# Optimization experiments

Measured on AMD Instinct MI355X. Metric: run time of the kernel, lower is better.

Reference implementation:

```python
import jax, jax.numpy as jnp
import numpy as np

H = 8          # heads
C = 128        # out_channels per head (hidden_dim)
EMB = 256      # embedding_dim
NG = 64        # number of graphs in batch
EPS_LN = 1e-5


def _layer_norm(x, g, b):
    mu = x.mean(-1, keepdims=True)
    var = ((x - mu) ** 2).mean(-1, keepdims=True)
    return (x - mu) * jax.lax.rsqrt(var + EPS_LN) * g + b


def _transformer_conv(x, src, dst, Wq, bq, Wk, bk, Wv, bv, Ws, bs, Wb):
    # PyG TransformerConv, heads=H, concat=False, beta=True, root_weight=True
    N = x.shape[0]
    q = (x @ Wq + bq).reshape(N, H, C)
    k = (x @ Wk + bk).reshape(N, H, C)
    v = (x @ Wv + bv).reshape(N, H, C)
    # per-edge attention logits: q_i . k_j / sqrt(C)   (i=dst, j=src)
    logits = jnp.einsum('ehc,ehc->eh', q[dst], k[src]) / jnp.sqrt(jnp.asarray(C, x.dtype))
    # segment softmax over incoming edges of each dst node
    m = jax.ops.segment_max(logits, dst, num_segments=N)
    m = jnp.where(jnp.isfinite(m), m, 0.0)
    ex = jnp.exp(logits - m[dst])
    den = jax.ops.segment_sum(ex, dst, num_segments=N)
    alpha = ex / (den[dst] + 1e-16)                      # [E,H]
    msg = alpha[:, :, None] * v[src]                     # [E,H,C]
    out = jax.ops.segment_sum(msg, dst, num_segments=N)  # [N,H,C]
    out = out.mean(axis=1)                               # concat=False -> head mean
    # beta-gated skip connection
    x_r = x @ Ws + bs                                    # [N,C]
    beta = jax.nn.sigmoid(jnp.concatenate([out, x_r, out - x_r], axis=-1) @ Wb)  # [N,1]
    return beta * x_r + (1.0 - beta) * out


def _lin(k, fan_in, fan_out, scale=None):
    s = scale if scale is not None else 1.0 / np.sqrt(fan_in)
    k1, k2 = jax.random.split(k)
    W = jax.random.uniform(k1, (fan_in, fan_out), jnp.float32, -s, s)
    b = jax.random.uniform(k2, (fan_out,), jnp.float32, -s, s)
    return W, b


def setup_inputs() -> dict:
    key = jax.random.key(0)
    ks = jax.random.split(key, 32)
    N, E, V = 50000, 400000, 10000
    inp = {
        'x': jax.random.randint(ks[0], (N,), 0, V, jnp.int32),
        'edge_index': jax.random.randint(ks[1], (2, E), 0, N, jnp.int32),
        'batch': jnp.sort(jax.random.randint(ks[2], (N,), 0, NG, jnp.int32)),
        'emb_w': jax.random.normal(ks[3], (V, EMB), jnp.float32),
    }
    ki = 4
    for l, din in enumerate([EMB, C]):
        Wq, bq = _lin(ks[ki], din, H * C); ki += 1
        Wk, bk = _lin(ks[ki], din, H * C); ki += 1
        Wv, bv = _lin(ks[ki], din, H * C); ki += 1
        Ws, bs = _lin(ks[ki], din, C); ki += 1
        Wb, _ = _lin(ks[ki], 3 * C, 1); ki += 1
        inp.update({f'Wq{l}': Wq, f'bq{l}': bq, f'Wk{l}': Wk, f'bk{l}': bk,
                    f'Wv{l}': Wv, f'bv{l}': bv, f'Ws{l}': Ws, f'bs{l}': bs,
                    f'Wb{l}': Wb, f'g{l}': jnp.ones((C,), jnp.float32),
                    f'be{l}': jnp.zeros((C,), jnp.float32)})
    Wc1, bc1 = _lin(ks[ki], C, C // 2); ki += 1
    Wc2, bc2 = _lin(ks[ki], C // 2, 1); ki += 1
    inp.update({'Wc1': Wc1, 'bc1': bc1, 'Wc2': Wc2, 'bc2': bc2})
    return inp


def reference(x, edge_index, batch, emb_w,
              Wq0, bq0, Wk0, bk0, Wv0, bv0, Ws0, bs0, Wb0, g0, be0,
              Wq1, bq1, Wk1, bk1, Wv1, bv1, Ws1, bs1, Wb1, g1, be1,
              Wc1, bc1, Wc2, bc2):
    src, dst = edge_index[0], edge_index[1]
    h = emb_w[x]                                           # [N, EMB]
    # layer 0 (no residual, per original `if i > 0`)
    h = _transformer_conv(h, src, dst, Wq0, bq0, Wk0, bk0, Wv0, bv0, Ws0, bs0, Wb0)
    h = jax.nn.relu(_layer_norm(h, g0, be0))               # dropout = identity (eval)
    # layer 1 (residual)
    res = h
    h = _transformer_conv(h, src, dst, Wq1, bq1, Wk1, bk1, Wv1, bv1, Ws1, bs1, Wb1)
    h = jax.nn.relu(_layer_norm(h + res, g1, be1))
    # global mean pool over graphs
    s = jax.ops.segment_sum(h, batch, num_segments=NG)     # [NG, C]
    cnt = jax.ops.segment_sum(jnp.ones((h.shape[0],), h.dtype), batch, num_segments=NG)
    pooled = s / jnp.maximum(cnt, 1.0)[:, None]
    # classifier MLP
    z = jax.nn.relu(pooled @ Wc1 + bc1)
    return z @ Wc2 + bc2                                   # [NG, 1]
```

## Files before the change

### kernel.cpp

```cpp
#include <hip/hip_runtime.h>
#include <hip/hip_fp16.h>
#include <math.h>

#define HEADS 8
#define CDIM 128
#define HC 1024
#define EMBD 256
#define NGRAPH 64
#define QSCALE 0.08838834764831845f
#define QSCALE2 0.12751744f

typedef unsigned short u16;
typedef short s8v __attribute__((ext_vector_type(8)));
typedef float f4v __attribute__((ext_vector_type(4)));
typedef _Float16 h2v __attribute__((ext_vector_type(2)));

__device__ __forceinline__ float b2f(u16 u) {
  union { unsigned int i; float f; } v; v.i = ((unsigned int)u) << 16; return v.f;
}
__device__ __forceinline__ u16 f2b(float f) {
  union { float f; unsigned int i; } v; v.f = f;
  unsigned int i = v.i;
  unsigned int r = (i + 0x7FFFu + ((i >> 16) & 1u)) >> 16;
  return (u16)r;
}
__device__ __forceinline__ u16 f2h(float f) {
  __half h = __float2half(f);
  return *(u16*)&h;
}

union U4H { uint4 u; h2v h[4]; };

__global__ __launch_bounds__(256) void embed_kernel(
    const int* __restrict__ x, const float* __restrict__ emb,
    u16* __restrict__ h0, int N)
{
  int idx = blockIdx.x * 256 + threadIdx.x;
  if (idx >= N * (EMBD / 4)) return;
  int n = idx >> 6;
  int j = (idx & 63) * 4;
  int vid = x[n];
  float4 f = *(const float4*)&emb[(size_t)vid * EMBD + j];
  ushort4 u;
  u.x = f2b(f.x); u.y = f2b(f.y); u.z = f2b(f.z); u.w = f2b(f.w);
  *(ushort4*)&h0[(size_t)n * EMBD + j] = u;
}

__global__ __launch_bounds__(256) void build_WsT_swz(
    const float* __restrict__ in, u16* __restrict__ out, int K)
{
  const int KS = K / 32;
  int nt = blockIdx.x;
  int ks = blockIdx.y;
  int t = threadIdx.x;
  int lane = t & 63, ni = t >> 6;
  int q4 = lane >> 4, cn = lane & 15;
  int colL = nt * 64 + ni * 16 + cn;
  int kbase = ks * 32 + q4 * 8;
  u16 tmp[8];
#pragma unroll
  for (int e8 = 0; e8 < 8; e8++) tmp[e8] = f2b(in[(size_t)(kbase + e8) * CDIM + colL]);
  size_t base = ((((size_t)nt * KS + ks) * 4 + ni) * 64 + lane) * 8;
  *(uint4*)&out[base] = *(uint4*)tmp;
}

__global__ __launch_bounds__(256) void build_qkvT_swz(
    const float* __restrict__ Wq, const float* __restrict__ Wk, const float* __restrict__ Wv,
    u16* __restrict__ WT, int K, int hpc)
{
  __shared__ u16 tile[64][130];
  const int KS = K / 32;
  int rg0 = blockIdx.x * 128;
  int kk0 = blockIdx.y * 64;
  int chunkCols = hpc * 384;
  int chunk = rg0 / chunkCols;
  int within = rg0 - chunk * chunkCols;
  int head = chunk * hpc + within / 384;
  int sub = within % 384;
  int sect = sub >> 7;
  const float* W = (sect == 0) ? Wq : (sect == 1 ? Wk : Wv);
  float scale = (sect == 0) ? QSCALE2 : 1.0f;
  int cc0 = head * CDIM;
  int t = threadIdx.x;
  int ci = t & 127, k2 = t >> 7;
#pragma unroll
  for (int ii = 0; ii < 32; ii++) {
    int ki = k2 + ii * 2;
    tile[ki][ci] = f2b(W[(size_t)(kk0 + ki) * HC + cc0 + ci] * scale);
  }
  __syncthreads();

  int lane = t & 63, ni = t >> 6;
  int q4 = lane >> 4, cn = lane & 15;
  int ntBase = rg0 >> 6;
#pragma unroll
  for (int ntd = 0; ntd < 2; ntd++) {
#pragma unroll
    for (int ksd = 0; ksd < 2; ksd++) {
      int colL = ntd * 64 + ni * 16 + cn;
      int kL = ksd * 32 + q4 * 8;
      u16 tmp[8];
#pragma unroll
      for (int e8 = 0; e8 < 8; e8++) tmp[e8] = tile[kL + e8][colL];
      size_t base = ((((size_t)(ntBase + ntd) * KS + (kk0 >> 5) + ksd) * 4 + ni) * 64 + lane) * 8;
      *(uint4*)&WT[base] = *(uint4*)tmp;
    }
  }
}
__global__ __launch_bounds__(256) void build_qkvb(
    const float* __restrict__ bq, const float* __restrict__ bk, const float* __restrict__ bv,
    float* __restrict__ bT, int hpc)
{
  int rg = blockIdx.x * 256 + threadIdx.x;
  if (rg >= 3 * HC) return;
  int chunkCols = hpc * 384;
  int chunk = rg / chunkCols;
  int within = rg - chunk * chunkCols;
  int head = chunk * hpc + within / 384;
  int sub = within % 384;
  int sect = sub >> 7;
  int cc = head * CDIM + (sub & 127);
  bT[rg] = (sect == 0) ? bq[cc] * QSCALE2 : (sect == 1 ? bk[cc] : bv[cc]);
}

__global__ __launch_bounds__(256) void deg_kernel(const int* __restrict__ ei, int* __restrict__ deg, int E) {
  int e = blockIdx.x * 256 + threadIdx.x;
  if (e < E) atomicAdd(&deg[ei[E + e]], 1);
}
__global__ __launch_bounds__(256) void scan1_kernel(const int* __restrict__ deg, int* __restrict__ row_ptr,
                                                    int* __restrict__ bsum, int N) {
  __shared__ int sb[256];
  int t = threadIdx.x, idx = blockIdx.x * 256 + t;
  int x = (idx < N) ? deg[idx] : 0;
  sb[t] = x; __syncthreads();
  for (int off = 1; off < 256; off <<= 1) {
    int y = (t >= off) ? sb[t - off] : 0;
    __syncthreads(); sb[t] += y; __syncthreads();
  }
  if (idx < N) row_ptr[idx + 1] = sb[t];
  if (t == 255) bsum[blockIdx.x] = sb[255];
  if (idx == 0) row_ptr[0] = 0;
}
__global__ __launch_bounds__(256) void scan2_kernel(int* __restrict__ bsum, int B) {
  __shared__ int sb[256];
  int t = threadIdx.x;
  int x = (t < B) ? bsum[t] : 0;
  sb[t] = x; __syncthreads();
  for (int off = 1; off < 256; off <<= 1) {
    int y = (t >= off) ? sb[t - off] : 0;
    __syncthreads(); sb[t] += y; __syncthreads();
  }
  if (t < B) bsum[t] = sb[t] - x;
}
__global__ __launch_bounds__(256) void scan3_kernel(int* __restrict__ row_ptr, const int* __restrict__ bsum, int N) {
  int idx = blockIdx.x * 256 + threadIdx.x;
  if (idx < N) row_ptr[idx + 1] += bsum[idx >> 8];
}
__global__ __launch_bounds__(256) void scatter_kernel(const int* __restrict__ ei,
                                                      const int* __restrict__ row_ptr,
                                                      int* __restrict__ fill, int* __restrict__ col, int E) {
  int e = blockIdx.x * 256 + threadIdx.x;
  if (e >= E) return;
  int d = ei[E + e];
  int pos = row_ptr[d] + atomicAdd(&fill[d], 1);
  col[pos] = ei[e];
}
__global__ void gb_kernel(const int* __restrict__ batch, int* __restrict__ gb, int N) {
  int g = threadIdx.x;
  if (g > NGRAPH) return;
  int lo = 0, hi = N;
  while (lo < hi) { int mid = (lo + hi) >> 1; if (batch[mid] < g) lo = mid + 1; else hi = mid; }
  gb[g] = lo;
}

template <int K, int F16OUT>
__global__ __launch_bounds__(256, 3) void gemm_lds(
    const u16* __restrict__ A, const u16* __restrict__ Bswz, int col0tile,
    const float* __restrict__ bias, u16* __restrict__ outT,
    int M, int Ncol)
{
  const int LDK = K + 8;
  const int KS = K / 32;
  __shared__ __align__(16) u16 As[64 * LDK];
  int t = threadIdx.x, lane = t & 63, w = t >> 6;
  int q4 = lane >> 4, cn = lane & 15;
  int m0 = blockIdx.y * 64;
  int ntL = blockIdx.x * 4 + w;
  bool wActive = ntL * 64 < Ncol;
  int ntG = col0tile + ntL;

  if (m0 + 64 <= M) {
    const u16* Ablk = A + (size_t)m0 * K;
#pragma unroll
    for (int ii = 0; ii < K / 32; ii++) {
      int g = (ii * 256 + t) * 8;
      int r = g / K, c = g - r * K;
      *(uint4*)&As[r * LDK + c] = *(const uint4*)(Ablk + g);
    }
  } else {
#pragma unroll
    for (int ii = 0; ii < K / 32; ii++) {
      int g = (ii * 256 + t) * 8;
      int r = g / K, c = g - r * K;
      int gr = m0 + r; if (gr >= M) gr = M - 1;
      *(uint4*)&As[r * LDK + c] = *(const uint4*)(A + (size_t)gr * K + c);
    }
  }
  __syncthreads();

  if (!wActive) return;

  f4v acc[4][4] = {};
  const u16* bb = Bswz + ((size_t)ntG * KS * 4) * 64 * 8 + lane * 8;
#pragma unroll
  for (int ks = 0; ks < KS; ks++) {
    s8v bf[4], af[4];
#pragma unroll
    for (int ni = 0; ni < 4; ni++)
      bf[ni] = *(const s8v*)(bb + ((size_t)ks * 4 + ni) * 64 * 8);
#pragma unroll
    for (int mi = 0; mi < 4; mi++)
      af[mi] = *(const s8v*)&As[(mi * 16 + cn) * LDK + ks * 32 + q4 * 8];
#pragma unroll
    for (int mi = 0; mi < 4; mi++)
#pragma unroll
      for (int ni = 0; ni < 4; ni++)
        acc[mi][ni] = __builtin_amdgcn_mfma_f32_16x16x32_bf16(af[mi], bf[ni], acc[mi][ni], 0, 0, 0);
  }

  u16* obase = outT + (size_t)ntL * M * 64;
  float bv[4];
#pragma unroll
  for (int ni = 0; ni < 4; ni++) bv[ni] = bias[ntG * 64 + ni * 16 + cn];
#pragma unroll
  for (int mi = 0; mi < 4; mi++) {
#pragma unroll
    for (int j = 0; j < 4; j++) {
      int gm = m0 + mi * 16 + q4 * 4 + j;
      if (gm < M) {
#pragma unroll
        for (int ni = 0; ni < 4; ni++) {
          float val = acc[mi][ni][j] + bv[ni];
          obase[(size_t)gm * 64 + ni * 16 + cn] = F16OUT ? f2h(val) : f2b(val);
        }
      }
    }
  }
}

template <int HPC>
__global__ __launch_bounds__(256) void attn_chunk_kernel(
    const u16* __restrict__ qkv,
    const int* __restrict__ row_ptr, const int* __restrict__ col,
    float* __restrict__ outacc, int N, int first)
{
  int t = threadIdx.x;
  int w = t >> 6, lane = t & 63;
  int g = lane >> 4, i = lane & 15;
  int n, j;
  if (HPC == 4)      { n = blockIdx.x;                 j = w; }
  else if (HPC == 2) { n = blockIdx.x * 2 + (w >> 1);  j = w & 1; }
  else               { n = blockIdx.x * 4 + w;         j = 0; }
  bool active = (HPC == 4) ? true : (n < N);

  int itile = i >> 3, ioff = (i & 7) * 8;
  const u16* qb = qkv + (size_t)(j * 6 + 0 + itile) * N * 64 + ioff;
  const u16* kb = qkv + (size_t)(j * 6 + 2 + itile) * N * 64 + ioff;
  const u16* vb = qkv + (size_t)(j * 6 + 4 + itile) * N * 64 + ioff;

  float acc[8] = {};
  float m = -INFINITY, l = 0.f;
  if (active) {
    U4H qu; qu.u = *(const uint4*)(qb + (size_t)n * 64);
    int e0 = row_ptr[n], e1 = row_ptr[n + 1];
    for (int eb = e0; eb < e1; eb += 8) {
      int egA = eb + g, egB = eb + 4 + g;
      bool vA = egA < e1, vB = egB < e1;
      int sA = col[vA ? egA : e1 - 1];
      int sB = col[vB ? egB : e1 - 1];
      U4H kuA, vuA, kuB, vuB;
      kuA.u = *(const uint4*)(kb + (size_t)sA * 64);
      kuB.u = *(const uint4*)(kb + (size_t)sB * 64);
      vuA.u = *(const uint4*)(vb + (size_t)sA * 64);
      vuB.u = *(const uint4*)(vb + (size_t)sB * 64);

      float pA, pB;
#if defined(__has_builtin) && __has_builtin(__builtin_amdgcn_fdot2)
      pA = __builtin_amdgcn_fdot2(kuA.h[0], qu.h[0], 0.f, false);
      pA = __builtin_amdgcn_fdot2(kuA.h[1], qu.h[1], pA, false);
      pA = __builtin_amdgcn_fdot2(kuA.h[2], qu.h[2], pA, false);
      pA = __builtin_amdgcn_fdot2(kuA.h[3], qu.h[3], pA, false);
      pB = __builtin_amdgcn_fdot2(kuB.h[0], qu.h[0], 0.f, false);
      pB = __builtin_amdgcn_fdot2(kuB.h[1], qu.h[1], pB, false);
      pB = __builtin_amdgcn_fdot2(kuB.h[2], qu.h[2], pB, false);
      pB = __builtin_amdgcn_fdot2(kuB.h[3], qu.h[3], pB, false);
#else
      pA = 0.f; pB = 0.f;
#pragma unroll
      for (int z = 0; z < 4; z++) {
        pA += (float)kuA.h[z][0] * (float)qu.h[z][0] + (float)kuA.h[z][1] * (float)qu.h[z][1];
        pB += (float)kuB.h[z][0] * (float)qu.h[z][0] + (float)kuB.h[z][1] * (float)qu.h[z][1];
      }
#endif
#pragma unroll
      for (int off = 1; off <= 8; off <<= 1) {
        pA += __shfl_xor(pA, off, 64);
        pB += __shfl_xor(pB, off, 64);
      }
      if (!vA) pA = -INFINITY;
      if (!vB) pB = -INFINITY;

      {
        float pm = fmaxf(pA, __shfl_xor(pA, 16));
        pm = fmaxf(pm, __shfl_xor(pm, 32));
        if (pm > m) {
          float al = exp2f(m - pm);
          l *= al;
#pragma unroll
          for (int z = 0; z < 8; z++) acc[z] *= al;
          m = pm;
        }
        float pe = exp2f(pA - m);
        float ps = pe + __shfl_xor(pe, 16);
        ps += __shfl_xor(ps, 32);
        l += ps;
#pragma unroll
        for (int z = 0; z < 4; z++) {
          acc[2 * z]     = fmaf(pe, (float)vuA.h[z][0], acc[2 * z]);
          acc[2 * z + 1] = fmaf(pe, (float)vuA.h[z][1], acc[2 * z + 1]);
        }
      }
      {
        float pm = fmaxf(pB, __shfl_xor(pB, 16));
        pm = fmaxf(pm, __shfl_xor(pm, 32));
        if (pm > m) {
          float al = exp2f(m - pm);
          l *= al;
#pragma unroll
          for (int z = 0; z < 8; z++) acc[z] *= al;
          m = pm;
        }
        float pe = exp2f(pB - m);
        float ps = pe + __shfl_xor(pe, 16);
        ps += __shfl_xor(ps, 32);
        l += ps;
#pragma unroll
        for (int z = 0; z < 4; z++) {
          acc[2 * z]     = fmaf(pe, (float)vuB.h[z][0], acc[2 * z]);
          acc[2 * z + 1] = fmaf(pe, (float)vuB.h[z][1], acc[2 * z + 1]);
        }
      }
    }
  }
  float inv = 0.125f / (l + 1e-16f);
#pragma unroll
  for (int z = 0; z < 8; z++) {
    float a = acc[z] * inv;
    a += __shfl_xor(a, 16);
    a += __shfl_xor(a, 32);
    acc[z] = a;
  }

  if (HPC == 1) {
    if (active && g == 0) {
      float* op = outacc + (size_t)n * CDIM + i * 8;
      if (first) {
        *(float4*)op       = make_float4(acc[0], acc[1], acc[2], acc[3]);
        *(float4*)(op + 4) = make_float4(acc[4], acc[5], acc[6], acc[7]);
      } else {
        float4 o0 = *(float4*)op, o1 = *(float4*)(op + 4);
        *(float4*)op       = make_float4(o0.x + acc[0], o0.y + acc[1], o0.z + acc[2], o0.w + acc[3]);
        *(float4*)(op + 4) = make_float4(o1.x + acc[4], o1.y + acc[5], o1.z + acc[6], o1.w + acc[7]);
      }
    }
  } else {
    __shared__ float sacc[4][128];
    if (g == 0) {
      *(float4*)&sacc[w][i * 8]     = make_float4(acc[0], acc[1], acc[2], acc[3]);
      *(float4*)&sacc[w][i * 8 + 4] = make_float4(acc[4], acc[5], acc[6], acc[7]);
    }
    __syncthreads();
    if (HPC == 4) {
      if (t < 128) {
        float v = sacc[0][t] + sacc[1][t] + sacc[2][t] + sacc[3][t];
        size_t o = (size_t)blockIdx.x * CDIM + t;
        outacc[o] = first ? v : (outacc[o] + v);
      }
    } else {
      int nn = blockIdx.x * 2 + (t >> 7);
      int c = t & 127;
      if (nn < N) {
        float v = sacc[(t >> 7) * 2][c] + sacc[(t >> 7) * 2 + 1][c];
        size_t o = (size_t)nn * CDIM + c;
        outacc[o] = first ? v : (outacc[o] + v);
      }
    }
  }
}

template <int LAYER>
__global__ __launch_bounds__(256) void epilogue_kernel(
    const float* __restrict__ outacc, const u16* __restrict__ xrT,
    const float* __restrict__ Wb, const float* __restrict__ gam, const float* __restrict__ bet,
    const u16* __restrict__ res,
    u16* __restrict__ hout,
    float* __restrict__ houtf,
    int N)
{
  int t = threadIdx.x;
  int local = t >> 7, c = t & 127, w = t >> 6;
  int n = blockIdx.x * 2 + local;
  bool act = n < N;
  __shared__ float sred[8];
  __shared__ float smv[2][3];

  float oc = 0.f, xc = 0.f;
  if (act) {
    oc = outacc[(size_t)n * CDIM + c];
    xc = b2f(xrT[((size_t)(c >> 6) * N + n) * 64 + (c & 63)]);
  }
  float pb = oc * Wb[c] + xc * Wb[CDIM + c] + (oc - xc) * Wb[2 * CDIM + c];
#pragma unroll
  for (int off = 32; off; off >>= 1) pb += __shfl_down(pb, off, 64);
  if ((t & 63) == 0) sred[w] = pb;
  __syncthreads();
  if (t == 0)   smv[0][0] = 1.f / (1.f + __expf(-(sred[0] + sred[1])));
  if (t == 128) smv[1][0] = 1.f / (1.f + __expf(-(sred[2] + sred[3])));
  __syncthreads();
  float beta = smv[local][0];
  float val = beta * xc + (1.f - beta) * oc;
  if (LAYER == 1 && act) val += b2f(res[(size_t)n * CDIM + c]);

  float s1 = val, s2 = val * val;
#pragma unroll
  for (int off = 32; off; off >>= 1) {
    s1 += __shfl_down(s1, off, 64);
    s2 += __shfl_down(s2, off, 64);
  }
  __syncthreads();
  if ((t & 63) == 0) { sred[w * 2] = s1; sred[w * 2 + 1] = s2; }
  __syncthreads();
  if (t == 0) {
    float S1 = sred[0] + sred[2], S2 = sred[1] + sred[3];
    float mu = S1 * (1.f / CDIM);
    float var = fmaxf(S2 * (1.f / CDIM) - mu * mu, 0.f);
    smv[0][1] = mu; smv[0][2] = 1.f / sqrtf(var + 1e-5f);
  }
  if (t == 128) {
    float S1 = sred[4] + sred[6], S2 = sred[5] + sred[7];
    float mu = S1 * (1.f / CDIM);
    float var = fmaxf(S2 * (1.f / CDIM) - mu * mu, 0.f);
    smv[1][1] = mu; smv[1][2] = 1.f / sqrtf(var + 1e-5f);
  }
  __syncthreads();
  if (act) {
    float y = (val - smv[local][1]) * smv[local][2] * gam[c] + bet[c];
    y = fmaxf(y, 0.f);
    if (LAYER == 0) hout[(size_t)n * CDIM + c] = f2b(y);
    else            houtf[(size_t)n * CDIM + c] = y;
  }
}

__global__ __launch_bounds__(256) void classifier_kernel(
    const float* __restrict__ hf, const int* __restrict__ gb,
    const float* __restrict__ Wc1, const float* __restrict__ bc1,
    const float* __restrict__ Wc2, const float* __restrict__ bc2,
    float* __restrict__ out)
{
  int g = blockIdx.x, t = threadIdx.x;
  int half = t >> 7, c = t & 127;
  int s = gb[g], e = gb[g + 1];
  float acc = 0.f;
  for (int n = s + half; n < e; n += 2) acc += hf[(size_t)n * CDIM + c];
  __shared__ float sb[2][128];
  __shared__ float sp[128], sz[64];
  sb[half][c] = acc;
  __syncthreads();
  float cg = fmaxf((float)(e - s), 1.f);
  if (t < 128) sp[t] = (sb[0][t] + sb[1][t]) / cg;
  __syncthreads();
  if (t < 64) {
    float a = bc1[t];
    for (int cc = 0; cc < 128; cc++) a += sp[cc] * Wc1[cc * 64 + t];
    sz[t] = fmaxf(a, 0.f);
  }
  __syncthreads();
  if (t < 64) {
    float pbv = sz[t] * Wc2[t];
    for (int off = 32; off; off >>= 1) pbv += __shfl_down(pbv, off, 64);
    if (t == 0) out[g] = pbv + bc2[0];
  }
}

extern "C" void kernel_launch(void* const* d_in, const int* in_sizes, int n_in,
                              void* d_out, int out_size, void* d_ws, size_t ws_size,
                              hipStream_t stream)
{
  if (n_in != 30) return;

  const int N = in_sizes[0];
  const int E = in_sizes[1] / 2;

  const int* x     = (const int*)d_in[0];
  const int* ei    = (const int*)d_in[1];
  const int* batch = (const int*)d_in[2];
  const float* emb = (const float*)d_in[3];
  const float* Wq0 = (const float*)d_in[4];  const float* bq0 = (const float*)d_in[5];
  const float* Wk0 = (const float*)d_in[6];  const float* bk0 = (const float*)d_in[7];
  const float* Wv0 = (const float*)d_in[8];  const float* bv0 = (const float*)d_in[9];
  const float* Ws0 = (const float*)d_in[10]; const float* bs0 = (const float*)d_in[11];
  const float* Wb0 = (const float*)d_in[12]; const float* g0  = (const float*)d_in[13]; const float* be0 = (const float*)d_in[14];
  const float* Wq1 = (const float*)d_in[15]; const float* bq1 = (const float*)d_in[16];
  const float* Wk1 = (const float*)d_in[17]; const float* bk1 = (const float*)d_in[18];
  const float* Wv1 = (const float*)d_in[19]; const float* bv1 = (const float*)d_in[20];
  const float* Ws1 = (const float*)d_in[21]; const float* bs1 = (const float*)d_in[22];
  const float* Wb1 = (const float*)d_in[23]; const float* g1  = (const float*)d_in[24]; const float* be1 = (const float*)d_in[25];
  const float* Wc1 = (const float*)d_in[26]; const float* bc1 = (const float*)d_in[27];
  const float* Wc2 = (const float*)d_in[28]; const float* bc2 = (const float*)d_in[29];

  auto rnd = [](size_t b) { return (b + 511) & ~(size_t)511; };
  size_t fixedBytes =
      rnd((size_t)N * CDIM * 4) +
      rnd((size_t)N * EMBD * 2) +
      rnd((size_t)N * CDIM * 2) * 2 +
      rnd((size_t)3 * HC * EMBD * 2) +
      rnd((size_t)3 * HC * CDIM * 2) +
      rnd((size_t)3 * HC * 4) * 2 +
      rnd((size_t)CDIM * EMBD * 2) +
      rnd((size_t)CDIM * CDIM * 2) +
      rnd((size_t)N * 4) * 2 +
      rnd((size_t)(N + 1) * 4) +
      rnd((size_t)E * 4) +
      rnd(256 * 4) +
      rnd(65 * 4);
  int hpc = 1;
  if (ws_size >= fixedBytes + rnd((size_t)N * 4 * 384 * 2)) hpc = 4;
  else if (ws_size >= fixedBytes + rnd((size_t)N * 2 * 384 * 2)) hpc = 2;
  const int chunkCols = hpc * 384;
  const int nchunks = HEADS / hpc;

  char* ws = (char*)d_ws;
  size_t off = 0;
  auto alloc = [&](size_t bytes) -> void* {
    void* p = ws + off;
    off += (bytes + 511) & ~(size_t)511;
    return p;
  };
  u16*   qkvc  = (u16*)  alloc((size_t)N * chunkCols * 2);
  float* outacc= (float*)alloc((size_t)N * CDIM * 4);
  u16*   h0    = (u16*)  alloc((size_t)N * EMBD * 2);
  u16*   h1    = (u16*)  alloc((size_t)N * CDIM * 2);
  u16*   xrb   = (u16*)  alloc((size_t)N * CDIM * 2);
  u16*   WT0   = (u16*)  alloc((size_t)3 * HC * EMBD * 2);
  u16*   WT1   = (u16*)  alloc((size_t)3 * HC * CDIM * 2);
  float* bT0   = (float*)alloc((size_t)3 * HC * 4);
  float* bT1   = (float*)alloc((size_t)3 * HC * 4);
  u16*   WsT0  = (u16*)  alloc((size_t)CDIM * EMBD * 2);
  u16*   WsT1  = (u16*)  alloc((size_t)CDIM * CDIM * 2);
  int*   deg   = (int*)  alloc((size_t)N * 4);
  int*   fill  = (int*)  alloc((size_t)N * 4);
  int*   rowp  = (int*)  alloc((size_t)(N + 1) * 4);
  int*   colb  = (int*)  alloc((size_t)E * 4);
  int*   bsum  = (int*)  alloc(256 * 4);
  int*   gb    = (int*)  alloc(65 * 4);

  hipMemsetAsync(deg, 0, (size_t)N * 4, stream);
  hipMemsetAsync(fill, 0, (size_t)N * 4, stream);

  embed_kernel<<<(N * 64 + 255) / 256, 256, 0, stream>>>(x, emb, h0, N);
  { dim3 gT(3 * HC / 128, EMBD / 64);
    build_qkvT_swz<<<gT, 256, 0, stream>>>(Wq0, Wk0, Wv0, WT0, EMBD, hpc); }
  { dim3 gT(3 * HC / 128, CDIM / 64);
    build_qkvT_swz<<<gT, 256, 0, stream>>>(Wq1, Wk1, Wv1, WT1, CDIM, hpc); }
  build_qkvb<<<(3 * HC + 255) / 256, 256, 0, stream>>>(bq0, bk0, bv0, bT0, hpc);
  build_qkvb<<<(3 * HC + 255) / 256, 256, 0, stream>>>(bq1, bk1, bv1, bT1, hpc);
  { dim3 gT(2, EMBD / 32);
    build_WsT_swz<<<gT, 256, 0, stream>>>(Ws0, WsT0, EMBD); }
  { dim3 gT(2, CDIM / 32);
    build_WsT_swz<<<gT, 256, 0, stream>>>(Ws1, WsT1, CDIM); }

  int nb = (N + 255) / 256;
  deg_kernel<<<(E + 255) / 256, 256, 0, stream>>>(ei, deg, E);
  scan1_kernel<<<nb, 256, 0, stream>>>(deg, rowp, bsum, N);
  scan2_kernel<<<1, 256, 0, stream>>>(bsum, nb);
  scan3_kernel<<<nb, 256, 0, stream>>>(rowp, bsum, N);
  scatter_kernel<<<(E + 255) / 256, 256, 0, stream>>>(ei, rowp, fill, colb, E);
  gb_kernel<<<1, 128, 0, stream>>>(batch, gb, N);

  int rowStrips = (N + 63) / 64;
  int attnBlocks = (hpc == 4) ? N : (hpc == 2 ? (N + 1) / 2 : (N + 3) / 4);
  int epiBlocks = (N + 1) / 2;

  for (int layer = 0; layer < 2; layer++) {
    const u16* Ain   = (layer == 0) ? h0 : h1;
    const u16* WT    = (layer == 0) ? WT0 : WT1;
    const float* bT  = (layer == 0) ? bT0 : bT1;
    const u16* WsT   = (layer == 0) ? WsT0 : WsT1;
    const float* bs  = (layer == 0) ? bs0 : bs1;
    const float* Wb  = (layer == 0) ? Wb0 : Wb1;
    const float* gam = (layer == 0) ? g0 : g1;
    const float* bet = (layer == 0) ? be0 : be1;
    int K = (layer == 0) ? EMBD : CDIM;

    dim3 gXR(1, rowStrips);
    dim3 gQKV((chunkCols + 255) / 256, rowStrips);
    if (K == EMBD) gemm_lds<EMBD, 0><<<gXR, 256, 0, stream>>>(Ain, WsT, 0, bs, xrb, N, CDIM);
    else           gemm_lds<CDIM, 0><<<gXR, 256, 0, stream>>>(Ain, WsT, 0, bs, xrb, N, CDIM);
    for (int c = 0; c < nchunks; c++) {
      int col0tile = c * (chunkCols / 64);
      if (K == EMBD)
        gemm_lds<EMBD, 1><<<gQKV, 256, 0, stream>>>(Ain, WT, col0tile, bT, qkvc, N, chunkCols);
      else
        gemm_lds<CDIM, 1><<<gQKV, 256, 0, stream>>>(Ain, WT, col0tile, bT, qkvc, N, chunkCols);
      int first = (c == 0) ? 1 : 0;
      if (hpc == 4)      attn_chunk_kernel<4><<<attnBlocks, 256, 0, stream>>>(qkvc, rowp, colb, outacc, N, first);
      else if (hpc == 2) attn_chunk_kernel<2><<<attnBlocks, 256, 0, stream>>>(qkvc, rowp, colb, outacc, N, first);
      else               attn_chunk_kernel<1><<<attnBlocks, 256, 0, stream>>>(qkvc, rowp, colb, outacc, N, first);
    }
    if (layer == 0) {
      epilogue_kernel<0><<<epiBlocks, 256, 0, stream>>>(outacc, xrb, Wb, gam, bet,
                                                        (const u16*)nullptr, h1, (float*)nullptr, N);
    } else {
      epilogue_kernel<1><<<epiBlocks, 256, 0, stream>>>(outacc, xrb, Wb, gam, bet,
                                                        h1, (u16*)nullptr, (float*)qkvc, N);
    }
  }

  classifier_kernel<<<NGRAPH, 256, 0, stream>>>((const float*)qkvc, gb, Wc1, bc1, Wc2, bc2,
                                                (float*)d_out);
}
```

Before: 1.137 ms.

## Fuse skip GEMM into QKV GEMM and epilogue into final attention chunk

On the default four-heads-per-chunk path, the skip projection GEMM is folded into the first QKV chunk GEMM as extra column tiles. The beta gate, residual add, layer norm and ReLU epilogue move into the last attention chunk kernel, which removes two launches per layer and one round trip of outacc. The online softmax now handles both edges of an iteration with one max and one sum reduction instead of two, cutting shuffles. The fused epilogue costs one 256-thread block per node with several barriers, and the final layer output now goes to h0 instead of qkvc.

```diff
diff --git a/kernel.cpp b/kernel.cpp
--- a/kernel.cpp
+++ b/kernel.cpp
@@ -173,11 +173,13 @@
   gb[g] = lo;
 }
 
-template <int K, int F16OUT>
+template <int K>
 __global__ __launch_bounds__(256, 3) void gemm_lds(
-    const u16* __restrict__ A, const u16* __restrict__ Bswz, int col0tile,
-    const float* __restrict__ bias, u16* __restrict__ outT,
-    int M, int Ncol)
+    const u16* __restrict__ A, const u16* __restrict__ Bq, const u16* __restrict__ Bx,
+    int col0tile, int xrTile0,
+    const float* __restrict__ biasQ, const float* __restrict__ biasX,
+    u16* __restrict__ outQ, u16* __restrict__ outX,
+    int M, int nTiles)
 {
   const int LDK = K + 8;
   const int KS = K / 32;
@@ -186,8 +188,9 @@
   int q4 = lane >> 4, cn = lane & 15;
   int m0 = blockIdx.y * 64;
   int ntL = blockIdx.x * 4 + w;
-  bool wActive = ntL * 64 < Ncol;
+  bool wActive = ntL < nTiles;
   int ntG = col0tile + ntL;
+  bool isXr = ntG >= xrTile0;
 
   if (m0 + 64 <= M) {
     const u16* Ablk = A + (size_t)m0 * K;
@@ -211,13 +214,15 @@
   if (!wActive) return;
 
   f4v acc[4][4] = {};
-  const u16* bb = Bswz + ((size_t)ntG * KS * 4) * 64 * 8 + lane * 8;
+  const u16* bb = isXr
+      ? Bx + ((size_t)(ntG - xrTile0) * KS * 4) * 512 + lane * 8
+      : Bq + ((size_t)ntG * KS * 4) * 512 + lane * 8;
 #pragma unroll
   for (int ks = 0; ks < KS; ks++) {
     s8v bf[4], af[4];
 #pragma unroll
     for (int ni = 0; ni < 4; ni++)
-      bf[ni] = *(const s8v*)(bb + ((size_t)ks * 4 + ni) * 64 * 8);
+      bf[ni] = *(const s8v*)(bb + ((size_t)ks * 4 + ni) * 512);
 #pragma unroll
     for (int mi = 0; mi < 4; mi++)
       af[mi] = *(const s8v*)&As[(mi * 16 + cn) * LDK + ks * 32 + q4 * 8];
@@ -228,10 +233,13 @@
         acc[mi][ni] = __builtin_amdgcn_mfma_f32_16x16x32_bf16(af[mi], bf[ni], acc[mi][ni], 0, 0, 0);
   }
 
-  u16* obase = outT + (size_t)ntL * M * 64;
+  u16* obase = isXr ? outX + (size_t)(ntG - xrTile0) * M * 64
+                    : outQ + (size_t)ntL * M * 64;
   float bv[4];
 #pragma unroll
-  for (int ni = 0; ni < 4; ni++) bv[ni] = bias[ntG * 64 + ni * 16 + cn];
+  for (int ni = 0; ni < 4; ni++)
+    bv[ni] = isXr ? biasX[(ntG - xrTile0) * 64 + ni * 16 + cn]
+                  : biasQ[ntG * 64 + ni * 16 + cn];
 #pragma unroll
   for (int mi = 0; mi < 4; mi++) {
 #pragma unroll
@@ -241,18 +249,21 @@
 #pragma unroll
         for (int ni = 0; ni < 4; ni++) {
           float val = acc[mi][ni][j] + bv[ni];
-          obase[(size_t)gm * 64 + ni * 16 + cn] = F16OUT ? f2h(val) : f2b(val);
+          obase[(size_t)gm * 64 + ni * 16 + cn] = isXr ? f2b(val) : f2h(val);
         }
       }
     }
   }
 }
 
-template <int HPC>
+template <int HPC, int LAST, int LAYER>
 __global__ __launch_bounds__(256) void attn_chunk_kernel(
     const u16* __restrict__ qkv,
     const int* __restrict__ row_ptr, const int* __restrict__ col,
-    float* __restrict__ outacc, int N, int first)
+    float* __restrict__ outacc, int N, int first,
+    const u16* __restrict__ xrT, const float* __restrict__ Wb,
+    const float* __restrict__ gam, const float* __restrict__ bet,
+    const u16* __restrict__ res, u16* __restrict__ hout, float* __restrict__ houtf)
 {
   int t = threadIdx.x;
   int w = t >> 6, lane = t & 63;
@@ -310,45 +321,31 @@
       if (!vA) pA = -INFINITY;
       if (!vB) pB = -INFINITY;
 
-      {
-        float pm = fmaxf(pA, __shfl_xor(pA, 16));
-        pm = fmaxf(pm, __shfl_xor(pm, 32));
-        if (pm > m) {
-          float al = exp2f(m - pm);
-          l *= al;
-#pragma unroll
-          for (int z = 0; z < 8; z++) acc[z] *= al;
-          m = pm;
-        }
-        float pe = exp2f(pA - m);
-        float ps = pe + __shfl_xor(pe, 16);
-        ps += __shfl_xor(ps, 32);
-        l += ps;
-#pragma unroll
-        for (int z = 0; z < 4; z++) {
-          acc[2 * z]     = fmaf(pe, (float)vuA.h[z][0], acc[2 * z]);
-          acc[2 * z + 1] = fmaf(pe, (float)vuA.h[z][1], acc[2 * z + 1]);
-        }
-      }
-      {
-        float pm = fmaxf(pB, __shfl_xor(pB, 16));
-        pm = fmaxf(pm, __shfl_xor(pm, 32));
-        if (pm > m) {
-          float al = exp2f(m - pm);
-          l *= al;
-#pragma unroll
-          for (int z = 0; z < 8; z++) acc[z] *= al;
-          m = pm;
-        }
-        float pe = exp2f(pB - m);
-        float ps = pe + __shfl_xor(pe, 16);
-        ps += __shfl_xor(ps, 32);
-        l += ps;
-#pragma unroll
-        for (int z = 0; z < 4; z++) {
-          acc[2 * z]     = fmaf(pe, (float)vuB.h[z][0], acc[2 * z]);
-          acc[2 * z + 1] = fmaf(pe, (float)vuB.h[z][1], acc[2 * z + 1]);
-        }
+      float pm = fmaxf(pA, pB);
+      pm = fmaxf(pm, __shfl_xor(pm, 16));
+      pm = fmaxf(pm, __shfl_xor(pm, 32));
+      if (pm > m) {
+        float al = exp2f(m - pm);
+        l *= al;
+#pragma unroll
+        for (int z = 0; z < 8; z++) acc[z] *= al;
+        m = pm;
+      }
+      float peA = exp2f(pA - m);
+      float peB = exp2f(pB - m);
+      float ps = peA + peB;
+      ps += __shfl_xor(ps, 16);
+      ps += __shfl_xor(ps, 32);
+      l += ps;
+#pragma unroll
+      for (int z = 0; z < 4; z++) {
+        acc[2 * z]     = fmaf(peA, (float)vuA.h[z][0], acc[2 * z]);
+        acc[2 * z + 1] = fmaf(peA, (float)vuA.h[z][1], acc[2 * z + 1]);
+      }
+#pragma unroll
+      for (int z = 0; z < 4; z++) {
+        acc[2 * z]     = fmaf(peB, (float)vuB.h[z][0], acc[2 * z]);
+        acc[2 * z + 1] = fmaf(peB, (float)vuB.h[z][1], acc[2 * z + 1]);
       }
     }
   }
@@ -380,7 +377,55 @@
       *(float4*)&sacc[w][i * 8 + 4] = make_float4(acc[4], acc[5], acc[6], acc[7]);
     }
     __syncthreads();
-    if (HPC == 4) {
+    if (HPC == 4 && LAST) {
+      __shared__ float sred[4];
+      __shared__ float smv[3];
+      int c = t;
+      float v = 0.f, xc = 0.f, pb = 0.f;
+      if (t < 128) {
+        v = sacc[0][t] + sacc[1][t] + sacc[2][t] + sacc[3][t];
+        if (!first) v += outacc[(size_t)n * CDIM + t];
+        xc = b2f(xrT[((size_t)(c >> 6) * N + n) * 64 + (c & 63)]);
+        pb = v * Wb[c] + xc * Wb[CDIM + c] + (v - xc) * Wb[2 * CDIM + c];
+      }
+#pragma unroll
+      for (int off = 32; off; off >>= 1) pb += __shfl_down(pb, off, 64);
+      if (t == 0)  sred[0] = pb;
+      if (t == 64) sred[1] = pb;
+      __syncthreads();
+      if (t == 0) smv[0] = 1.f / (1.f + __expf(-(sred[0] + sred[1])));
+      __syncthreads();
+      float beta = smv[0];
+      float val = 0.f;
+      if (t < 128) {
+        val = beta * xc + (1.f - beta) * v;
+        if (LAYER == 1) val += b2f(res[(size_t)n * CDIM + c]);
+      }
+      float s1 = (t < 128) ? val : 0.f;
+      float s2 = (t < 128) ? val * val : 0.f;
+#pragma unroll
+      for (int off = 32; off; off >>= 1) {
+        s1 += __shfl_down(s1, off, 64);
+        s2 += __shfl_down(s2, off, 64);
+      }
+      __syncthreads();
+      if (t == 0)  { sred[0] = s1; sred[1] = s2; }
+      if (t == 64) { sred[2] = s1; sred[3] = s2; }
+      __syncthreads();
+      if (t == 0) {
+        float S1 = sred[0] + sred[2], S2 = sred[1] + sred[3];
+        float mu = S1 * (1.f / CDIM);
+        float var = fmaxf(S2 * (1.f / CDIM) - mu * mu, 0.f);
+        smv[1] = mu; smv[2] = 1.f / sqrtf(var + 1e-5f);
+      }
+      __syncthreads();
+      if (t < 128) {
+        float y = (val - smv[1]) * smv[2] * gam[c] + bet[c];
+        y = fmaxf(y, 0.f);
+        if (LAYER == 0) hout[(size_t)n * CDIM + c] = f2b(y);
+        else            houtf[(size_t)n * CDIM + c] = y;
+      }
+    } else if (HPC == 4) {
       if (t < 128) {
         float v = sacc[0][t] + sacc[1][t] + sacc[2][t] + sacc[3][t];
         size_t o = (size_t)blockIdx.x * CDIM + t;
@@ -403,9 +448,7 @@
     const float* __restrict__ outacc, const u16* __restrict__ xrT,
     const float* __restrict__ Wb, const float* __restrict__ gam, const float* __restrict__ bet,
     const u16* __restrict__ res,
-    u16* __restrict__ hout,
-    float* __restrict__ houtf,
-    int N)
+    u16* __restrict__ hout, float* __restrict__ houtf, int N)
 {
   int t = threadIdx.x;
   int local = t >> 7, c = t & 127, w = t >> 6;
@@ -538,6 +581,7 @@
   else if (ws_size >= fixedBytes + rnd((size_t)N * 2 * 384 * 2)) hpc = 2;
   const int chunkCols = hpc * 384;
   const int nchunks = HEADS / hpc;
+  const int qkvTiles = chunkCols / 64;
 
   char* ws = (char*)d_ws;
   size_t off = 0;
@@ -588,44 +632,81 @@
   gb_kernel<<<1, 128, 0, stream>>>(batch, gb, N);
 
   int rowStrips = (N + 63) / 64;
-  int attnBlocks = (hpc == 4) ? N : (hpc == 2 ? (N + 1) / 2 : (N + 3) / 4);
-  int epiBlocks = (N + 1) / 2;
-
-  for (int layer = 0; layer < 2; layer++) {
-    const u16* Ain   = (layer == 0) ? h0 : h1;
-    const u16* WT    = (layer == 0) ? WT0 : WT1;
-    const float* bT  = (layer == 0) ? bT0 : bT1;
-    const u16* WsT   = (layer == 0) ? WsT0 : WsT1;
-    const float* bs  = (layer == 0) ? bs0 : bs1;
-    const float* Wb  = (layer == 0) ? Wb0 : Wb1;
-    const float* gam = (layer == 0) ? g0 : g1;
-    const float* bet = (layer == 0) ? be0 : be1;
-    int K = (layer == 0) ? EMBD : CDIM;
-
-    dim3 gXR(1, rowStrips);
-    dim3 gQKV((chunkCols + 255) / 256, rowStrips);
-    if (K == EMBD) gemm_lds<EMBD, 0><<<gXR, 256, 0, stream>>>(Ain, WsT, 0, bs, xrb, N, CDIM);
-    else           gemm_lds<CDIM, 0><<<gXR, 256, 0, stream>>>(Ain, WsT, 0, bs, xrb, N, CDIM);
-    for (int c = 0; c < nchunks; c++) {
-      int col0tile = c * (chunkCols / 64);
+  float* hfinal = (float*)h0;
+
+  if (hpc == 4) {
+    for (int layer = 0; layer < 2; layer++) {
+      const u16* Ain   = (layer == 0) ? h0 : h1;
+      const u16* WT    = (layer == 0) ? WT0 : WT1;
+      const float* bT  = (layer == 0) ? bT0 : bT1;
+      const u16* WsT   = (layer == 0) ? WsT0 : WsT1;
+      const float* bs  = (layer == 0) ? bs0 : bs1;
+      const float* Wb  = (layer == 0) ? Wb0 : Wb1;
+      const float* gam = (layer == 0) ? g0 : g1;
+      const float* bet = (layer == 0) ? be0 : be1;
+      int K = (layer == 0) ? EMBD : CDIM;
+
+      int nT0 = qkvTiles + 2;
+      dim3 gG0((nT0 + 3) / 4, rowStrips);
+      dim3 gG1((qkvTiles + 3) / 4, rowStrips);
       if (K == EMBD)
-        gemm_lds<EMBD, 1><<<gQKV, 256, 0, stream>>>(Ain, WT, col0tile, bT, qkvc, N, chunkCols);
+        gemm_lds<EMBD><<<gG0, 256, 0, stream>>>(Ain, WT, WsT, 0, qkvTiles, bT, bs, qkvc, xrb, N, nT0);
       else
-        gemm_lds<CDIM, 1><<<gQKV, 256, 0, stream>>>(Ain, WT, col0tile, bT, qkvc, N, chunkCols);
-      int first = (c == 0) ? 1 : 0;
-      if (hpc == 4)      attn_chunk_kernel<4><<<attnBlocks, 256, 0, stream>>>(qkvc, rowp, colb, outacc, N, first);
-      else if (hpc == 2) attn_chunk_kernel<2><<<attnBlocks, 256, 0, stream>>>(qkvc, rowp, colb, outacc, N, first);
-      else               attn_chunk_kernel<1><<<attnBlocks, 256, 0, stream>>>(qkvc, rowp, colb, outacc, N, first);
-    }
-    if (layer == 0) {
-      epilogue_kernel<0><<<epiBlocks, 256, 0, stream>>>(outacc, xrb, Wb, gam, bet,
-                                                        (const u16*)nullptr, h1, (float*)nullptr, N);
-    } else {
-      epilogue_kernel<1><<<epiBlocks, 256, 0, stream>>>(outacc, xrb, Wb, gam, bet,
-                                                        h1, (u16*)nullptr, (float*)qkvc, N);
-    }
-  }
-
-  classifier_kernel<<<NGRAPH, 256, 0, stream>>>((const float*)qkvc, gb, Wc1, bc1, Wc2, bc2,
+        gemm_lds<CDIM><<<gG0, 256, 0, stream>>>(Ain, WT, WsT, 0, qkvTiles, bT, bs, qkvc, xrb, N, nT0);
+      attn_chunk_kernel<4, 0, 0><<<N, 256, 0, stream>>>(qkvc, rowp, colb, outacc, N, 1,
+          nullptr, nullptr, nullptr, nullptr, nullptr, nullptr, nullptr);
+      if (K == EMBD)
+        gemm_lds<EMBD><<<gG1, 256, 0, stream>>>(Ain, WT, WsT, qkvTiles, 1 << 30, bT, bs, qkvc, xrb, N, qkvTiles);
+      else
+        gemm_lds<CDIM><<<gG1, 256, 0, stream>>>(Ain, WT, WsT, qkvTiles, 1 << 30, bT, bs, qkvc, xrb, N, qkvTiles);
+      if (layer == 0)
+        attn_chunk_kernel<4, 1, 0><<<N, 256, 0, stream>>>(qkvc, rowp, colb, outacc, N, 0,
+            xrb, Wb, gam, bet, nullptr, h1, nullptr);
+      else
+        attn_chunk_kernel<4, 1, 1><<<N, 256, 0, stream>>>(qkvc, rowp, colb, outacc, N, 0,
+            xrb, Wb, gam, bet, h1, nullptr, hfinal);
+    }
+  } else {
+    int attnBlocks = (hpc == 2) ? (N + 1) / 2 : (N + 3) / 4;
+    int epiBlocks = (N + 1) / 2;
+    for (int layer = 0; layer < 2; layer++) {
+      const u16* Ain   = (layer == 0) ? h0 : h1;
+      const u16* WT    = (layer == 0) ? WT0 : WT1;
+      const float* bT  = (layer == 0) ? bT0 : bT1;
+      const u16* WsT   = (layer == 0) ? WsT0 : WsT1;
+      const float* bs  = (layer == 0) ? bs0 : bs1;
+      const float* Wb  = (layer == 0) ? Wb0 : Wb1;
+      const float* gam = (layer == 0) ? g0 : g1;
+      const float* bet = (layer == 0) ? be0 : be1;
+      int K = (layer == 0) ? EMBD : CDIM;
+
+      dim3 gXR(1, rowStrips);
+      dim3 gQKV((qkvTiles + 3) / 4, rowStrips);
+      if (K == EMBD) gemm_lds<EMBD><<<gXR, 256, 0, stream>>>(Ain, WT, WsT, 0, 0, bT, bs, qkvc, xrb, N, 2);
+      else           gemm_lds<CDIM><<<gXR, 256, 0, stream>>>(Ain, WT, WsT, 0, 0, bT, bs, qkvc, xrb, N, 2);
+      for (int c = 0; c < nchunks; c++) {
+        int col0tile = c * qkvTiles;
+        if (K == EMBD)
+          gemm_lds<EMBD><<<gQKV, 256, 0, stream>>>(Ain, WT, WsT, col0tile, 1 << 30, bT, bs, qkvc, xrb, N, qkvTiles);
+        else
+          gemm_lds<CDIM><<<gQKV, 256, 0, stream>>>(Ain, WT, WsT, col0tile, 1 << 30, bT, bs, qkvc, xrb, N, qkvTiles);
+        int first = (c == 0) ? 1 : 0;
+        if (hpc == 2)
+          attn_chunk_kernel<2, 0, 0><<<attnBlocks, 256, 0, stream>>>(qkvc, rowp, colb, outacc, N, first,
+              nullptr, nullptr, nullptr, nullptr, nullptr, nullptr, nullptr);
+        else
+          attn_chunk_kernel<1, 0, 0><<<attnBlocks, 256, 0, stream>>>(qkvc, rowp, colb, outacc, N, first,
+              nullptr, nullptr, nullptr, nullptr, nullptr, nullptr, nullptr);
+      }
+      if (layer == 0)
+        epilogue_kernel<0><<<epiBlocks, 256, 0, stream>>>(outacc, xrb, Wb, gam, bet,
+                                                          (const u16*)nullptr, h1, (float*)nullptr, N);
+      else
+        epilogue_kernel<1><<<epiBlocks, 256, 0, stream>>>(outacc, xrb, Wb, gam, bet,
+                                                          h1, (u16*)nullptr, hfinal, N);
+    }
+  }
+
+  classifier_kernel<<<NGRAPH, 256, 0, stream>>>(hfinal, gb, Wc1, bc1, Wc2, bc2,
                                                 (float*)d_out);
 }
```

Measured after the change: 1.098 ms. 3.5% less time.
